# Kernel optimization log

Measured on AMD Instinct MI355X. Metric: run time of the kernel, lower is better.

The kernel has to match this reference:

```python
import jax, jax.numpy as jnp
import numpy as np

L, B, N, D, H = 4, 4, 2048, 512, 8
HD = D // H  # head dim 64
EPS = 1e-5

def setup_inputs() -> dict:
    key = jax.random.key(0)
    ks = jax.random.split(key, 8)
    s = 0.02  # init scale for weights
    f32 = jnp.float32
    return {
        "x": jax.random.normal(ks[0], (B, N, D), f32),
        "Wq": jax.random.normal(ks[1], (L, D, D), f32) * s,
        "Wk": jax.random.normal(ks[2], (L, D, D), f32) * s,
        "Wv": jax.random.normal(ks[3], (L, D, D), f32) * s,
        "Wo": jax.random.normal(ks[4], (L, D, D), f32) * s,
        "bo": jnp.zeros((L, D), f32),
        "ln1_g": jnp.ones((L, D), f32),
        "ln1_b": jnp.zeros((L, D), f32),
        "W1": jax.random.normal(ks[5], (L, D, D), f32) * s,
        "b1": jnp.zeros((L, D), f32),
        "W2": jax.random.normal(ks[6], (L, D, D), f32) * s,
        "b2": jnp.zeros((L, D), f32),
        "ln2_g": jnp.ones((L, D), f32),
        "ln2_b": jnp.zeros((L, D), f32),
    }

def _layernorm(x, g, b):
    mu = jnp.mean(x, axis=-1, keepdims=True)
    var = jnp.mean(jnp.square(x - mu), axis=-1, keepdims=True)
    return (x - mu) * jax.lax.rsqrt(var + EPS) * g + b

def reference(x, Wq, Wk, Wv, Wo, bo, ln1_g, ln1_b, W1, b1, W2, b2, ln2_g, ln2_b):
    scale = D ** -0.5  # dim1 == dim on the cfg=None path

    def layer(h, p):
        wq, wk, wv, wo, bo_, g1, bb1, w1, bh1, w2, bh2, g2, bb2 = p
        # --- Residual(PreNorm(Attention)) ---
        y = _layernorm(h, g1, bb1)
        def split_heads(t):  # [B,N,D] -> [B,H,N,HD]
            return t.reshape(B, N, H, HD).transpose(0, 2, 1, 3)
        q = split_heads(y @ wq)
        k = split_heads(y @ wk)
        v = split_heads(y @ wv)
        dots = jnp.einsum('bhid,bhjd->bhij', q, k) * scale
        attn = jax.nn.softmax(dots, axis=-1)
        o = jnp.einsum('bhij,bhjd->bhid', attn, v)
        o = o.transpose(0, 2, 1, 3).reshape(B, N, D)
        h = h + o @ wo + bo_
        # --- Residual(PreNorm(FeedForward)) ---
        y = _layernorm(h, g2, bb2)
        y = jax.nn.gelu(y @ w1 + bh1, approximate=False)
        h = h + y @ w2 + bh2
        return h, None

    params = (Wq, Wk, Wv, Wo, bo, ln1_g, ln1_b, W1, b1, W2, b2, ln2_g, ln2_b)
    out, _ = jax.lax.scan(layer, x, params)
    return out
```

## Files before the change

kernel.cpp:

```cpp
#include <hip/hip_runtime.h>
#include <hip/hip_bf16.h>


typedef __bf16 bf16x8 __attribute__((ext_vector_type(8)));
typedef float f32x4 __attribute__((ext_vector_type(4)));
typedef unsigned int u32x4 __attribute__((ext_vector_type(4)));
typedef unsigned int u32x2 __attribute__((ext_vector_type(2)));
typedef unsigned short u16;

__device__ __forceinline__ u16 f2b(float f) {
  unsigned int u; __builtin_memcpy(&u, &f, 4);
  u += 0x7fffu + ((u >> 16) & 1u);
  return (u16)(u >> 16);
}
__device__ __forceinline__ bf16x8 ld8(const u16* p) {
  u32x4 t = *(const u32x4*)p;
  bf16x8 r; __builtin_memcpy(&r, &t, 16); return r;
}
__device__ __forceinline__ unsigned pkhi(float a, float b) {
  unsigned ua, ub; __builtin_memcpy(&ua, &a, 4); __builtin_memcpy(&ub, &b, 4);
  return __builtin_amdgcn_perm(ua, ub, 0x07060302u);
}

#define GLL(gp, lp) __builtin_amdgcn_global_load_lds( \
    (const __attribute__((address_space(1))) void*)(gp), \
    (__attribute__((address_space(3))) void*)(lp), 16, 0, 0)

__device__ __forceinline__ int swz(int r) { return (r + (r >> 2)) & 3; }

__global__ __launch_bounds__(256) void tr_all_k(
    const float* __restrict__ Wq, const float* __restrict__ Wk,
    const float* __restrict__ Wv, const float* __restrict__ Wo,
    const float* __restrict__ W1, const float* __restrict__ W2,
    u16* __restrict__ wtqkv, u16* __restrict__ wto,
    u16* __restrict__ wt1, u16* __restrict__ wt2) {
  __shared__ float t[32][33];
  int tx = threadIdx.x, ty = threadIdx.y;
  int z = blockIdx.z, which = z >> 2, l = z & 3;
  const float* in;
  u16* out;
  switch (which) {
    case 0: in = Wq; out = wtqkv + l * 786432; break;
    case 1: in = Wk; out = wtqkv + l * 786432 + 262144; break;
    case 2: in = Wv; out = wtqkv + l * 786432 + 524288; break;
    case 3: in = Wo; out = wto + l * 262144; break;
    case 4: in = W1; out = wt1 + l * 262144; break;
    default: in = W2; out = wt2 + l * 262144; break;
  }
  int k0 = blockIdx.y * 32, n0 = blockIdx.x * 32;
  const float* ip = in + l * 262144;
#pragma unroll
  for (int i = 0; i < 4; i++)
    t[ty + i * 8][tx] = ip[(k0 + ty + i * 8) * 512 + n0 + tx];
  __syncthreads();
#pragma unroll
  for (int i = 0; i < 4; i++)
    out[(n0 + ty + i * 8) * 512 + k0 + tx] = f2b(t[tx][ty + i * 8]);
}

__global__ __launch_bounds__(256) void ln_k(const float* __restrict__ h,
                                            const float* __restrict__ gg,
                                            const float* __restrict__ bb,
                                            u16* __restrict__ y) {
  int tid = threadIdx.x, wave = tid >> 6, lane = tid & 63;
  int tok = blockIdx.x * 4 + wave;
  const float* hp = h + (size_t)tok * 512 + lane * 8;
  float x[8];
  *(float4*)&x[0] = *(const float4*)hp;
  *(float4*)&x[4] = *(const float4*)(hp + 4);
  float s = 0.f, ss = 0.f;
#pragma unroll
  for (int i = 0; i < 8; i++) { s += x[i]; ss += x[i] * x[i]; }
#pragma unroll
  for (int off = 1; off < 64; off <<= 1) {
    s += __shfl_xor(s, off, 64);
    ss += __shfl_xor(ss, off, 64);
  }
  float mean = s * (1.0f / 512.0f);
  float var = ss * (1.0f / 512.0f) - mean * mean;
  float rstd = rsqrtf(var + 1e-5f);
  u32x4 ov;
#pragma unroll
  for (int i = 0; i < 4; i++) {
    int d0 = lane * 8 + i * 2;
    float y0 = (x[i * 2]     - mean) * rstd * gg[d0]     + bb[d0];
    float y1 = (x[i * 2 + 1] - mean) * rstd * gg[d0 + 1] + bb[d0 + 1];
    ov[i] = (unsigned)f2b(y0) | ((unsigned)f2b(y1) << 16);
  }
  *(u32x4*)&y[(size_t)tok * 512 + lane * 8] = ov;
}

enum { EPI_RES = 1, EPI_GELU = 2 };

template <int EPI>
__global__ __launch_bounds__(512, 4) void gemm2_k(
    const u16* __restrict__ A, const u16* __restrict__ Bt,
    const float* __restrict__ bias, u16* __restrict__ out0,
    const float* __restrict__ hin, float* __restrict__ hout,
    float* __restrict__ fout) {
  __shared__ __align__(16) u16 As[3][64 * 64];
  __shared__ __align__(16) u16 Bs[3][128 * 64];
  const int tid = threadIdx.x;
  const int wave = tid >> 6, lane = tid & 63;
  const int quad = lane >> 4, l16 = lane & 15;
  const int wm = wave >> 2, wn = wave & 3;
  const int m0 = blockIdx.x * 64;
  const int n0 = blockIdx.y * 128;
  const int mb = m0 + wm * 32, nb = n0 + wn * 32;

  float hr[2][2][4];
  if constexpr (EPI == EPI_RES) {
#pragma unroll
    for (int mi = 0; mi < 2; ++mi)
#pragma unroll
      for (int ni = 0; ni < 2; ++ni) {
        int r0 = mb + mi * 16 + quad * 4, c = nb + ni * 16 + l16;
#pragma unroll
        for (int g = 0; g < 4; ++g)
          hr[mi][ni][g] = hin[(size_t)(r0 + g) * 512 + c];
      }
  }

  f32x4 acc[2][2];
#pragma unroll
  for (int i = 0; i < 2; i++)
#pragma unroll
    for (int j = 0; j < 2; j++) acc[i][j] = f32x4{0.f, 0.f, 0.f, 0.f};

  const int rowA = tid >> 3, cgA = (tid & 7) ^ (rowA & 7);
  const size_t agl = (size_t)(m0 + rowA) * 512 + cgA * 8;
  int rowB[2], cgB[2];
#pragma unroll
  for (int rnd = 0; rnd < 2; ++rnd) {
    int s = rnd * 512 + tid;
    rowB[rnd] = s >> 3;
    cgB[rnd] = (tid & 7) ^ (rowB[rnd] & 7);
  }
  const size_t bgl0 = (size_t)(n0 + rowB[0]) * 512 + cgB[0] * 8;
  const size_t bgl1 = (size_t)(n0 + rowB[1]) * 512 + cgB[1] * 8;

  int kbA[2][2], kbB[2][2];
#pragma unroll
  for (int mi = 0; mi < 2; ++mi) {
    int r = wm * 32 + mi * 16 + l16;
#pragma unroll
    for (int ks = 0; ks < 2; ++ks)
      kbA[mi][ks] = r * 64 + ((ks * 4 + quad) ^ (r & 7)) * 8;
  }
#pragma unroll
  for (int ni = 0; ni < 2; ++ni) {
    int r = wn * 32 + ni * 16 + l16;
#pragma unroll
    for (int ks = 0; ks < 2; ++ks)
      kbB[ni][ks] = r * 64 + ((ks * 4 + quad) ^ (r & 7)) * 8;
  }

  GLL(A + agl, &As[0][(wave * 64) * 8]);
  GLL(Bt + bgl0, &Bs[0][(wave * 64) * 8]);
  GLL(Bt + bgl1, &Bs[0][(512 + wave * 64) * 8]);
  GLL(A + agl + 64, &As[1][(wave * 64) * 8]);
  GLL(Bt + bgl0 + 64, &Bs[1][(wave * 64) * 8]);
  GLL(Bt + bgl1 + 64, &Bs[1][(512 + wave * 64) * 8]);

#pragma unroll
  for (int kt = 0; kt < 8; ++kt) {
    if (kt < 7) {
      asm volatile("s_waitcnt vmcnt(3)" ::: "memory");
    } else {
      asm volatile("s_waitcnt vmcnt(0)" ::: "memory");
    }
    __builtin_amdgcn_sched_barrier(0);
    __builtin_amdgcn_s_barrier();
    __builtin_amdgcn_sched_barrier(0);

    const u16* AsB = As[kt % 3];
    const u16* BsB = Bs[kt % 3];
    if (kt + 2 < 8) {
      u16* AsN = (u16*)As[(kt + 2) % 3];
      u16* BsN = (u16*)Bs[(kt + 2) % 3];
      const int k2 = (kt + 2) * 64;
      GLL(A + agl + k2, AsN + (wave * 64) * 8);
      GLL(Bt + bgl0 + k2, BsN + (wave * 64) * 8);
      GLL(Bt + bgl1 + k2, BsN + (512 + wave * 64) * 8);
    }

#pragma unroll
    for (int ks = 0; ks < 2; ++ks) {
      bf16x8 af[2], bf_[2];
#pragma unroll
      for (int mi = 0; mi < 2; ++mi) af[mi] = ld8(AsB + kbA[mi][ks]);
#pragma unroll
      for (int ni = 0; ni < 2; ++ni) bf_[ni] = ld8(BsB + kbB[ni][ks]);
#pragma unroll
      for (int mi = 0; mi < 2; ++mi)
#pragma unroll
        for (int ni = 0; ni < 2; ++ni)
          acc[mi][ni] = __builtin_amdgcn_mfma_f32_16x16x32_bf16(
              af[mi], bf_[ni], acc[mi][ni], 0, 0, 0);
    }
  }

#pragma unroll
  for (int mi = 0; mi < 2; ++mi) {
#pragma unroll
    for (int ni = 0; ni < 2; ++ni) {
      f32x4 a = acc[mi][ni];
      int r0 = mb + mi * 16 + quad * 4;
      int c = nb + ni * 16 + l16;
      float bi = bias[c];
      if constexpr (EPI == EPI_RES) {
#pragma unroll
        for (int g = 0; g < 4; ++g) {
          float v = hr[mi][ni][g] + a[g] + bi;
          if (hout) hout[(size_t)(r0 + g) * 512 + c] = v;
          if (fout) fout[(size_t)(r0 + g) * 512 + c] = v;
        }
      } else {
#pragma unroll
        for (int g = 0; g < 4; ++g) {
          float t = a[g] + bi;
          float gl = 0.5f * t * (1.0f + erff(t * 0.70710678118654752f));
          out0[(size_t)(r0 + g) * 512 + c] = f2b(gl);
        }
      }
    }
  }
}

__global__ __launch_bounds__(512, 6) void gemm_qkv_k(
    const u16* __restrict__ A, const u16* __restrict__ Bt,
    u16* __restrict__ outq, u16* __restrict__ outk, u16* __restrict__ outvt) {
  __shared__ __align__(16) u16 As[2][64 * 64];
  __shared__ __align__(16) u16 Bs[2][128 * 64];
  const int tid = threadIdx.x;
  const int wave = tid >> 6, lane = tid & 63;
  const int quad = lane >> 4, l16 = lane & 15;
  const int wm = wave >> 2, wn = wave & 3;
  const int m0 = blockIdx.x * 64;
  const int n0 = blockIdx.y * 128;
  const int mb = m0 + wm * 32, nb = n0 + wn * 32;

  f32x4 acc[2][2];
#pragma unroll
  for (int i = 0; i < 2; i++)
#pragma unroll
    for (int j = 0; j < 2; j++) acc[i][j] = f32x4{0.f, 0.f, 0.f, 0.f};

  const int rowA = tid >> 3, cgA = (tid & 7) ^ (rowA & 7);
  const size_t agl = (size_t)(m0 + rowA) * 512 + cgA * 8;
  int rowB[2], cgB[2];
#pragma unroll
  for (int rnd = 0; rnd < 2; ++rnd) {
    int s = rnd * 512 + tid;
    rowB[rnd] = s >> 3;
    cgB[rnd] = (tid & 7) ^ (rowB[rnd] & 7);
  }
  const size_t bgl0 = (size_t)(n0 + rowB[0]) * 512 + cgB[0] * 8;
  const size_t bgl1 = (size_t)(n0 + rowB[1]) * 512 + cgB[1] * 8;

  int kbA[2][2], kbB[2][2];
#pragma unroll
  for (int mi = 0; mi < 2; ++mi) {
    int r = wm * 32 + mi * 16 + l16;
#pragma unroll
    for (int ks = 0; ks < 2; ++ks)
      kbA[mi][ks] = r * 64 + ((ks * 4 + quad) ^ (r & 7)) * 8;
  }
#pragma unroll
  for (int ni = 0; ni < 2; ++ni) {
    int r = wn * 32 + ni * 16 + l16;
#pragma unroll
    for (int ks = 0; ks < 2; ++ks)
      kbB[ni][ks] = r * 64 + ((ks * 4 + quad) ^ (r & 7)) * 8;
  }

  GLL(A + agl, &As[0][(wave * 64) * 8]);
  GLL(Bt + bgl0, &Bs[0][(wave * 64) * 8]);
  GLL(Bt + bgl1, &Bs[0][(512 + wave * 64) * 8]);

#pragma unroll 2
  for (int kt = 0; kt < 8; ++kt) {
    __syncthreads();
    const u16* AsB = As[kt & 1];
    const u16* BsB = Bs[kt & 1];
    if (kt + 1 < 8) {
      u16* AsN = (u16*)As[(kt & 1) ^ 1];
      u16* BsN = (u16*)Bs[(kt & 1) ^ 1];
      const int k1 = (kt + 1) * 64;
      GLL(A + agl + k1, AsN + (wave * 64) * 8);
      GLL(Bt + bgl0 + k1, BsN + (wave * 64) * 8);
      GLL(Bt + bgl1 + k1, BsN + (512 + wave * 64) * 8);
    }

#pragma unroll
    for (int ks = 0; ks < 2; ++ks) {
      bf16x8 af[2], bf_[2];
#pragma unroll
      for (int mi = 0; mi < 2; ++mi) af[mi] = ld8(AsB + kbA[mi][ks]);
#pragma unroll
      for (int ni = 0; ni < 2; ++ni) bf_[ni] = ld8(BsB + kbB[ni][ks]);
#pragma unroll
      for (int mi = 0; mi < 2; ++mi)
#pragma unroll
        for (int ni = 0; ni < 2; ++ni)
          acc[mi][ni] = __builtin_amdgcn_mfma_f32_16x16x32_bf16(
              af[mi], bf_[ni], acc[mi][ni], 0, 0, 0);
    }
  }

#pragma unroll
  for (int mi = 0; mi < 2; ++mi) {
#pragma unroll
    for (int ni = 0; ni < 2; ++ni) {
      f32x4 a = acc[mi][ni];
      int r0 = mb + mi * 16 + quad * 4;
      int c = nb + ni * 16 + l16;
      if (c < 512) {
        const float C2 = 0.06375871506958306f;
#pragma unroll
        for (int g = 0; g < 4; ++g) outq[(size_t)(r0 + g) * 512 + c] = f2b(a[g] * C2);
      } else if (c < 1024) {
#pragma unroll
        for (int g = 0; g < 4; ++g) outk[(size_t)(r0 + g) * 512 + (c - 512)] = f2b(a[g]);
      } else {
        int cv = c - 1024, hh = cv >> 6, dd = cv & 63;
        int bb = r0 >> 11, nt = r0 & 2047;
        u32x2 pk;
        pk[0] = (unsigned)f2b(a[0]) | ((unsigned)f2b(a[1]) << 16);
        pk[1] = (unsigned)f2b(a[2]) | ((unsigned)f2b(a[3]) << 16);
        *(u32x2*)&outvt[((size_t)(bb * 8 + hh) * 64 + dd) * 2048 + nt] = pk;
      }
    }
  }
}

__global__ __launch_bounds__(256, 4) void attn_k(const u16* __restrict__ q,
                                                 const u16* __restrict__ k,
                                                 const u16* __restrict__ vt,
                                                 u16* __restrict__ o) {
  __shared__ __align__(16) u16 Ks[2][64 * 64];
  __shared__ __align__(16) u16 Vs[2][64 * 64];
  __shared__ float Lr[4][32];
  const int tid = threadIdx.x, wave = tid >> 6, lane = tid & 63;
  const int quad = lane >> 4, l16 = lane & 15;
  const int swl = l16 & 7;
  const int qh2 = wave & 1, kvs = wave >> 1;
  const int bh = blockIdx.x, b = bh >> 3, h = bh & 7;
  const int qt0 = blockIdx.y * 64;

  const u16* qpb = q + (size_t)(b * 2048 + qt0 + qh2 * 32) * 512 + h * 64;
  bf16x8 aq[2][2];
#pragma unroll
  for (int qt = 0; qt < 2; ++qt) {
    const u16* qp = qpb + (size_t)(qt * 16 + l16) * 512;
    aq[qt][0] = ld8(qp + quad * 8);
    aq[qt][1] = ld8(qp + 32 + quad * 8);
  }

  const u16* kp = k + (size_t)b * 2048 * 512 + h * 64;
  const u16* vp = vt + (size_t)bh * 64 * 2048;

  const int srow = lane >> 3, schk = lane & 7, sgc = schk ^ srow;
  const int krow0 = wave * 8 + srow;
  const size_t kgl0 = (size_t)krow0 * 512 + sgc * 8;
  const size_t kgl1 = (size_t)(krow0 + 32) * 512 + sgc * 8;
  const size_t vgl0 = (size_t)krow0 * 2048 + sgc * 8;
  const size_t vgl1 = (size_t)(krow0 + 32) * 2048 + sgc * 8;

  int kb[2][2];
#pragma unroll
  for (int t = 0; t < 2; ++t) {
    kb[t][0] = (kvs * 32 + t * 16 + l16) * 64 + ((quad)     ^ swl) * 8;
    kb[t][1] = (kvs * 32 + t * 16 + l16) * 64 + ((4 + quad) ^ swl) * 8;
  }
  const int vblo = l16 * 64 + (((kvs << 2) + (quad >> 1)) ^ swl) * 8 + (quad & 1) * 4;
  const int vbhi = l16 * 64 + (((kvs << 2) + 2 + (quad >> 1)) ^ swl) * 8 + (quad & 1) * 4;

  f32x4 oacc[4][2];
#pragma unroll
  for (int i = 0; i < 4; i++)
#pragma unroll
    for (int j = 0; j < 2; j++) oacc[i][j] = f32x4{0.f, 0.f, 0.f, 0.f};
  f32x4 lsacc[2];
  lsacc[0] = f32x4{0.f, 0.f, 0.f, 0.f};
  lsacc[1] = f32x4{0.f, 0.f, 0.f, 0.f};

  u32x4 onesw;
  onesw[0] = 0x3F803F80u; onesw[1] = 0x3F803F80u;
  onesw[2] = 0x3F803F80u; onesw[3] = 0x3F803F80u;
  bf16x8 onesf; __builtin_memcpy(&onesf, &onesw, 16);

  GLL(kp + kgl0, &Ks[0][(wave * 8) * 64]);
  GLL(kp + kgl1, &Ks[0][(32 + wave * 8) * 64]);
  GLL(vp + vgl0, &Vs[0][(wave * 8) * 64]);
  GLL(vp + vgl1, &Vs[0][(32 + wave * 8) * 64]);

#pragma unroll 2
  for (int kt = 0; kt < 32; ++kt) {
    __syncthreads();
    const u16* KsB = Ks[kt & 1];
    const u16* VsB = Vs[kt & 1];
    if (kt + 1 < 32) {
      u16* KsN = (u16*)Ks[(kt & 1) ^ 1];
      u16* VsN = (u16*)Vs[(kt & 1) ^ 1];
      const u16* kpn = kp + (size_t)(kt + 1) * 32768;
      const u16* vpn = vp + (size_t)(kt + 1) * 64;
      GLL(kpn + kgl0, KsN + (wave * 8) * 64);
      GLL(kpn + kgl1, KsN + (32 + wave * 8) * 64);
      GLL(vpn + vgl0, VsN + (wave * 8) * 64);
      GLL(vpn + vgl1, VsN + (32 + wave * 8) * 64);
    }

    bf16x8 kf[2][2];
#pragma unroll
    for (int t = 0; t < 2; ++t) {
      kf[t][0] = ld8(KsB + kb[t][0]);
      kf[t][1] = ld8(KsB + kb[t][1]);
    }
    f32x4 sa[2][2];
    __builtin_amdgcn_s_setprio(1);
#pragma unroll
    for (int t = 0; t < 2; ++t)
#pragma unroll
      for (int qt = 0; qt < 2; ++qt) {
        f32x4 z = f32x4{0.f, 0.f, 0.f, 0.f};
        z = __builtin_amdgcn_mfma_f32_16x16x32_bf16(kf[t][0], aq[qt][0], z, 0, 0, 0);
        z = __builtin_amdgcn_mfma_f32_16x16x32_bf16(kf[t][1], aq[qt][1], z, 0, 0, 0);
        sa[t][qt] = z;
      }
    __builtin_amdgcn_s_setprio(0);

    u32x4 pw[2];
#pragma unroll
    for (int t = 0; t < 2; ++t)
#pragma unroll
      for (int qt = 0; qt < 2; ++qt) {
        float p0 = __builtin_amdgcn_exp2f(sa[t][qt][0]);
        float p1 = __builtin_amdgcn_exp2f(sa[t][qt][1]);
        float p2 = __builtin_amdgcn_exp2f(sa[t][qt][2]);
        float p3 = __builtin_amdgcn_exp2f(sa[t][qt][3]);
        pw[qt][t * 2]     = pkhi(p1, p0);
        pw[qt][t * 2 + 1] = pkhi(p3, p2);
      }
    bf16x8 pf[2];
    __builtin_memcpy(&pf[0], &pw[0], 16);
    __builtin_memcpy(&pf[1], &pw[1], 16);

    __builtin_amdgcn_s_setprio(1);
#pragma unroll
    for (int dt = 0; dt < 4; ++dt) {
      u32x2 lo = *(const u32x2*)(VsB + vblo + dt * 1024);
      u32x2 hi = *(const u32x2*)(VsB + vbhi + dt * 1024);
      u32x4 w;
      w[0] = lo[0]; w[1] = lo[1]; w[2] = hi[0]; w[3] = hi[1];
      bf16x8 av; __builtin_memcpy(&av, &w, 16);
#pragma unroll
      for (int qt = 0; qt < 2; ++qt)
        oacc[dt][qt] = __builtin_amdgcn_mfma_f32_16x16x32_bf16(
            av, pf[qt], oacc[dt][qt], 0, 0, 0);
    }
#pragma unroll
    for (int qt = 0; qt < 2; ++qt)
      lsacc[qt] = __builtin_amdgcn_mfma_f32_16x16x32_bf16(
          onesf, pf[qt], lsacc[qt], 0, 0, 0);
    __builtin_amdgcn_s_setprio(0);
  }

  if (quad == 0) {
#pragma unroll
    for (int qt = 0; qt < 2; ++qt) Lr[wave][qt * 16 + l16] = lsacc[qt][0];
  }
  __syncthreads();

  float* R = (float*)&Ks[0][0];
  const int l7 = lane & 7;
  if (wave >= 2) {
    float* Rw = R + (wave - 2) * 2048;
#pragma unroll
    for (int dt = 0; dt < 4; ++dt)
#pragma unroll
      for (int qt = 0; qt < 2; ++qt) {
        int s = (dt * 2 + qt) ^ l7;
        *(f32x4*)&Rw[lane * 32 + s * 4] = oacc[dt][qt];
      }
  }
  __syncthreads();
  if (wave < 2) {
    float* Rw = R + wave * 2048;
    float inv[2];
#pragma unroll
    for (int qt = 0; qt < 2; ++qt)
      inv[qt] = 1.0f / (Lr[wave][qt * 16 + l16] + Lr[wave + 2][qt * 16 + l16]);
#pragma unroll
    for (int dt = 0; dt < 4; ++dt)
#pragma unroll
      for (int qt = 0; qt < 2; ++qt) {
        int s = (dt * 2 + qt) ^ l7;
        f32x4 v = *(f32x4*)&Rw[lane * 32 + s * 4];
        float i4 = inv[qt];
        float o0 = (oacc[dt][qt][0] + v[0]) * i4;
        float o1 = (oacc[dt][qt][1] + v[1]) * i4;
        float o2 = (oacc[dt][qt][2] + v[2]) * i4;
        float o3 = (oacc[dt][qt][3] + v[3]) * i4;
        u16* op = o + (size_t)(b * 2048 + qt0 + wave * 32 + qt * 16 + l16) * 512 +
                  h * 64 + dt * 16 + quad * 4;
        u32x2 pk;
        pk[0] = (unsigned)f2b(o0) | ((unsigned)f2b(o1) << 16);
        pk[1] = (unsigned)f2b(o2) | ((unsigned)f2b(o3) << 16);
        *(u32x2*)op = pk;
      }
  }
}

extern "C" void kernel_launch(void* const* d_in, const int* in_sizes, int n_in,
                              void* d_out, int out_size, void* d_ws,
                              size_t ws_size, hipStream_t stream) {
  const float* x   = (const float*)d_in[0];
  const float* Wq  = (const float*)d_in[1];
  const float* Wk  = (const float*)d_in[2];
  const float* Wv  = (const float*)d_in[3];
  const float* Wo  = (const float*)d_in[4];
  const float* bo  = (const float*)d_in[5];
  const float* g1  = (const float*)d_in[6];
  const float* bg1 = (const float*)d_in[7];
  const float* W1  = (const float*)d_in[8];
  const float* b1  = (const float*)d_in[9];
  const float* W2  = (const float*)d_in[10];
  const float* b2  = (const float*)d_in[11];
  const float* g2  = (const float*)d_in[12];
  const float* bg2 = (const float*)d_in[13];

  char* ws = (char*)d_ws;
  float* h    = (float*)ws;
  u16* yb     = (u16*)(ws + (16ll << 20));
  u16* qb     = (u16*)(ws + (24ll << 20));
  u16* kb     = (u16*)(ws + (32ll << 20));
  u16* vtb    = (u16*)(ws + (40ll << 20));
  u16* ob     = (u16*)(ws + (48ll << 20));
  u16* wtqkv  = (u16*)(ws + (56ll << 20));
  u16* wto    = (u16*)(ws + (62ll << 20));
  u16* wt1    = (u16*)(ws + (64ll << 20));
  u16* wt2    = (u16*)(ws + (66ll << 20));

  tr_all_k<<<dim3(16, 16, 24), dim3(32, 8), 0, stream>>>(
      Wq, Wk, Wv, Wo, W1, W2, wtqkv, wto, wt1, wt2);

  for (int l = 0; l < 4; ++l) {
    const float* hsrc = (l == 0) ? x : h;
    ln_k<<<2048, 256, 0, stream>>>(hsrc, g1 + l * 512, bg1 + l * 512, yb);
    gemm_qkv_k<<<dim3(128, 12), 512, 0, stream>>>(
        yb, wtqkv + l * 786432, qb, kb, vtb);
    attn_k<<<dim3(32, 32), 256, 0, stream>>>(qb, kb, vtb, ob);
    gemm2_k<EPI_RES><<<dim3(128, 4), 512, 0, stream>>>(
        ob, wto + l * 262144, bo + l * 512, nullptr, hsrc, h, nullptr);
    ln_k<<<2048, 256, 0, stream>>>(h, g2 + l * 512, bg2 + l * 512, yb);
    gemm2_k<EPI_GELU><<<dim3(128, 4), 512, 0, stream>>>(
        yb, wt1 + l * 262144, b1 + l * 512, qb, nullptr, nullptr, nullptr);
    gemm2_k<EPI_RES><<<dim3(128, 4), 512, 0, stream>>>(
        qb, wt2 + l * 262144, b2 + l * 512, nullptr, h,
        (l == 3) ? nullptr : h, (l == 3) ? (float*)d_out : nullptr);
  }
}
```

Baseline: 545.6 us.

## Deepen QKV GEMM pipeline to four-stage K=32 ring with explicit vmcnt waits

Restructures the QKV projection GEMM's shared-memory staging from a two-buffer K=64 scheme into a four-buffer K=32 ring. Loads are issued two tiles ahead, and each iteration waits with a targeted s_waitcnt vmcnt instead of a full __syncthreads drain. The goal is to keep more global-to-LDS loads in flight and overlap them with MFMA work. In exchange it doubles the number of barriers per tile and relies on hand-counted outstanding loads per wave, which is fragile. It also uses a swz() helper assumed to exist elsewhere in the file.

```diff
diff --git a/kernel.cpp b/kernel.cpp
--- a/kernel.cpp
+++ b/kernel.cpp
@@ -230,8 +230,8 @@
 __global__ __launch_bounds__(512, 6) void gemm_qkv_k(
     const u16* __restrict__ A, const u16* __restrict__ Bt,
     u16* __restrict__ outq, u16* __restrict__ outk, u16* __restrict__ outvt) {
-  __shared__ __align__(16) u16 As[2][64 * 64];
-  __shared__ __align__(16) u16 Bs[2][128 * 64];
+  __shared__ __align__(16) u16 As[4][64 * 32];
+  __shared__ __align__(16) u16 Bs[4][128 * 32];
   const int tid = threadIdx.x;
   const int wave = tid >> 6, lane = tid & 63;
   const int quad = lane >> 4, l16 = lane & 15;
@@ -246,66 +246,64 @@
 #pragma unroll
     for (int j = 0; j < 2; j++) acc[i][j] = f32x4{0.f, 0.f, 0.f, 0.f};
 
-  const int rowA = tid >> 3, cgA = (tid & 7) ^ (rowA & 7);
+  const int rowA = (tid & 255) >> 2, cgA = (tid & 3) ^ swz(rowA);
   const size_t agl = (size_t)(m0 + rowA) * 512 + cgA * 8;
-  int rowB[2], cgB[2];
-#pragma unroll
-  for (int rnd = 0; rnd < 2; ++rnd) {
-    int s = rnd * 512 + tid;
-    rowB[rnd] = s >> 3;
-    cgB[rnd] = (tid & 7) ^ (rowB[rnd] & 7);
-  }
-  const size_t bgl0 = (size_t)(n0 + rowB[0]) * 512 + cgB[0] * 8;
-  const size_t bgl1 = (size_t)(n0 + rowB[1]) * 512 + cgB[1] * 8;
-
-  int kbA[2][2], kbB[2][2];
+  const int rowB = tid >> 2, cgB = (tid & 3) ^ swz(rowB);
+  const size_t bgl = (size_t)(n0 + rowB) * 512 + cgB * 8;
+
+  int kbA[2], kbB[2];
 #pragma unroll
   for (int mi = 0; mi < 2; ++mi) {
     int r = wm * 32 + mi * 16 + l16;
-#pragma unroll
-    for (int ks = 0; ks < 2; ++ks)
-      kbA[mi][ks] = r * 64 + ((ks * 4 + quad) ^ (r & 7)) * 8;
+    kbA[mi] = r * 32 + (quad ^ swz(r)) * 8;
   }
 #pragma unroll
   for (int ni = 0; ni < 2; ++ni) {
     int r = wn * 32 + ni * 16 + l16;
-#pragma unroll
-    for (int ks = 0; ks < 2; ++ks)
-      kbB[ni][ks] = r * 64 + ((ks * 4 + quad) ^ (r & 7)) * 8;
-  }
-
-  GLL(A + agl, &As[0][(wave * 64) * 8]);
-  GLL(Bt + bgl0, &Bs[0][(wave * 64) * 8]);
-  GLL(Bt + bgl1, &Bs[0][(512 + wave * 64) * 8]);
-
-#pragma unroll 2
-  for (int kt = 0; kt < 8; ++kt) {
-    __syncthreads();
-    const u16* AsB = As[kt & 1];
-    const u16* BsB = Bs[kt & 1];
-    if (kt + 1 < 8) {
-      u16* AsN = (u16*)As[(kt & 1) ^ 1];
-      u16* BsN = (u16*)Bs[(kt & 1) ^ 1];
-      const int k1 = (kt + 1) * 64;
-      GLL(A + agl + k1, AsN + (wave * 64) * 8);
-      GLL(Bt + bgl0 + k1, BsN + (wave * 64) * 8);
-      GLL(Bt + bgl1 + k1, BsN + (512 + wave * 64) * 8);
-    }
-
-#pragma unroll
-    for (int ks = 0; ks < 2; ++ks) {
-      bf16x8 af[2], bf_[2];
-#pragma unroll
-      for (int mi = 0; mi < 2; ++mi) af[mi] = ld8(AsB + kbA[mi][ks]);
-#pragma unroll
-      for (int ni = 0; ni < 2; ++ni) bf_[ni] = ld8(BsB + kbB[ni][ks]);
-#pragma unroll
-      for (int mi = 0; mi < 2; ++mi)
-#pragma unroll
-        for (int ni = 0; ni < 2; ++ni)
-          acc[mi][ni] = __builtin_amdgcn_mfma_f32_16x16x32_bf16(
-              af[mi], bf_[ni], acc[mi][ni], 0, 0, 0);
-    }
+    kbB[ni] = r * 32 + (quad ^ swz(r)) * 8;
+  }
+
+  if (tid < 256) GLL(A + agl, &As[0][(wave * 64) * 8]);
+  GLL(Bt + bgl, &Bs[0][(wave * 64) * 8]);
+  if (tid < 256) GLL(A + agl + 32, &As[1][(wave * 64) * 8]);
+  GLL(Bt + bgl + 32, &Bs[1][(wave * 64) * 8]);
+
+#pragma unroll
+  for (int kt = 0; kt < 16; ++kt) {
+    if (kt < 15) {
+      if (wave < 4) {
+        asm volatile("s_waitcnt vmcnt(2)" ::: "memory");
+      } else {
+        asm volatile("s_waitcnt vmcnt(1)" ::: "memory");
+      }
+    } else {
+      asm volatile("s_waitcnt vmcnt(0)" ::: "memory");
+    }
+    __builtin_amdgcn_sched_barrier(0);
+    __builtin_amdgcn_s_barrier();
+    __builtin_amdgcn_sched_barrier(0);
+
+    const u16* AsB = As[kt & 3];
+    const u16* BsB = Bs[kt & 3];
+    if (kt + 2 < 16) {
+      u16* AsN = (u16*)As[(kt + 2) & 3];
+      u16* BsN = (u16*)Bs[(kt + 2) & 3];
+      const int k2 = (kt + 2) * 32;
+      if (tid < 256) GLL(A + agl + k2, AsN + (wave * 64) * 8);
+      GLL(Bt + bgl + k2, BsN + (wave * 64) * 8);
+    }
+
+    bf16x8 af[2], bf_[2];
+#pragma unroll
+    for (int mi = 0; mi < 2; ++mi) af[mi] = ld8(AsB + kbA[mi]);
+#pragma unroll
+    for (int ni = 0; ni < 2; ++ni) bf_[ni] = ld8(BsB + kbB[ni]);
+#pragma unroll
+    for (int mi = 0; mi < 2; ++mi)
+#pragma unroll
+      for (int ni = 0; ni < 2; ++ni)
+        acc[mi][ni] = __builtin_amdgcn_mfma_f32_16x16x32_bf16(
+            af[mi], bf_[ni], acc[mi][ni], 0, 0, 0);
   }
 
 #pragma unroll
```

Measured after the change: 529.7 us. 1.03x faster.
